# Optimization experiments

Measured on AMD Instinct MI355X. Metric: run time of the kernel, lower is better.

The kernel has to match this reference:

```python
import jax, jax.numpy as jnp
import numpy as np

N_QUBITS = 10
N_LAYERS = 4
DIM = 1 << N_QUBITS            # 1024
N3 = 3 * N_QUBITS              # params per rotation layer
N_PARAM = N3 * (N_LAYERS + 1)  # 150
BATCH = 8192

_C64 = jnp.complex64


def _rx(t):
    c = jnp.cos(t / 2).astype(_C64)
    s = jnp.sin(t / 2).astype(_C64)
    return jnp.stack([jnp.stack([c, -1j * s]), jnp.stack([-1j * s, c])])


def _ry(t):
    c = jnp.cos(t / 2).astype(_C64)
    s = jnp.sin(t / 2).astype(_C64)
    return jnp.stack([jnp.stack([c, -s]), jnp.stack([s, c])])


def _rz(t):
    e = jnp.exp(-1j * t.astype(_C64) / 2)
    z = jnp.zeros((), _C64)
    return jnp.stack([jnp.stack([e, z]), jnp.stack([z, jnp.conj(e)])])


def _apply1(state, gate, wire):
    """Apply a 2x2 gate to qubit `wire` of state [B, 2, ..., 2]."""
    axis = wire + 1  # axis 0 is batch
    s = jnp.moveaxis(state, axis, -1)
    s = jnp.einsum('ij,...j->...i', gate, s)
    return jnp.moveaxis(s, -1, axis)


def _cnot(state, ctrl, tgt):
    a, b = ctrl + 1, tgt + 1
    s = jnp.moveaxis(state, (a, b), (-2, -1))  # [..., ctrl, tgt]
    s = jnp.stack([s[..., 0, :], s[..., 1, ::-1]], axis=-2)
    return jnp.moveaxis(s, (-2, -1), (a, b))


def setup_inputs() -> dict:
    key = jax.random.key(0)
    k1, k2 = jax.random.split(key)
    x = jax.random.normal(k1, (BATCH, DIM), dtype=jnp.float32)
    he_std = (2.0 ** 0.5) * (5.0 ** -0.5)  # gain * 5^-0.5, w_mul with lrmul=1
    weight = jax.random.uniform(k2, (N_PARAM,), minval=0.0,
                                maxval=2.0 * np.pi, dtype=jnp.float32) * he_std
    return {"x": x, "weight": weight}


def reference(x, weight):
    # encoding layer: L2-normalize then cast to complex amplitudes
    norm = jnp.linalg.norm(x, axis=-1, keepdims=True)
    s = (x / jnp.maximum(norm, 1e-12)).astype(_C64)
    s = s.reshape((x.shape[0],) + (2,) * N_QUBITS)

    for l in range(N_LAYERS):
        w = weight[l * N3:(l + 1) * N3]
        # XYZ layer: Rx, then Ry, then Rz on every qubit
        for q in range(N_QUBITS):
            s = _apply1(s, _rx(w[q]), q)
        for q in range(N_QUBITS):
            s = _apply1(s, _ry(w[N_QUBITS + q]), q)
        for q in range(N_QUBITS):
            s = _apply1(s, _rz(w[2 * N_QUBITS + q]), q)
        # ring of CNOTs
        for q in range(N_QUBITS):
            s = _cnot(s, q, (q + 1) % N_QUBITS)

    # final YZY layer
    w = weight[N_LAYERS * N3:]
    for q in range(N_QUBITS):
        s = _apply1(s, _ry(w[q]), q)
    for q in range(N_QUBITS):
        s = _apply1(s, _rz(w[N_QUBITS + q]), q)
    for q in range(N_QUBITS):
        s = _apply1(s, _ry(w[2 * N_QUBITS + q]), q)

    return s.reshape(x.shape[0], 1, DIM).real
```

## Files before the change

kernel.cpp:

```cpp
#include <hip/hip_runtime.h>
#include <stdint.h>

typedef uint16_t u16;
typedef __attribute__((ext_vector_type(2))) float f32x2;
typedef __attribute__((ext_vector_type(4))) float f32x4;
typedef __attribute__((ext_vector_type(8))) short short8;
typedef __attribute__((ext_vector_type(4))) float float4v;
typedef __attribute__((ext_vector_type(4))) uint16_t u16x4;
typedef __attribute__((ext_vector_type(8))) uint16_t u16x8;

#define DIMQ 1024
#define BATCH 8192
#define KDIM 1024
#define NDIM 1024

#define RDL(v, l) __int_as_float(__builtin_amdgcn_readlane(__float_as_int(v), (l)))

__device__ __forceinline__ u16 f2bf(float f) {
  uint32_t u = __float_as_uint(f);
  u += 0x7fffu + ((u >> 16) & 1u);
  return (u16)(u >> 16);
}

template<int MASK>
__device__ __forceinline__ float lane_xor(float x) {
  if constexpr (MASK == 1)
    return __int_as_float(__builtin_amdgcn_update_dpp(0, __float_as_int(x), 0xB1, 0xF, 0xF, true));
  else if constexpr (MASK == 2)
    return __int_as_float(__builtin_amdgcn_update_dpp(0, __float_as_int(x), 0x4E, 0xF, 0xF, true));
  else if constexpr (MASK == 8)
    return __int_as_float(__builtin_amdgcn_update_dpp(0, __float_as_int(x), 0x128, 0xF, 0xF, true));
  else if constexpr (MASK == 4)
    return __int_as_float(__builtin_amdgcn_ds_swizzle(__float_as_int(x), 0x101F));
  else if constexpr (MASK == 16)
    return __int_as_float(__builtin_amdgcn_ds_swizzle(__float_as_int(x), 0x401F));
  else
    return __shfl_xor(x, 32, 64);
}

template<int MASK>
__device__ __forceinline__ void lane_gate8(float* ar, float* ai, int lane,
    float u00r, float u00i, float u01r, float u01i,
    float u10r, float u10i, float u11r, float u11i) {
  bool hi = (lane & MASK) != 0;
  float cmr = hi ? u11r : u00r, cmi = hi ? u11i : u00i;
  float cor = hi ? u10r : u01r, coi = hi ? u10i : u01i;
  float otr[8], oti[8];
#pragma unroll
  for (int r = 0; r < 8; ++r) otr[r] = lane_xor<MASK>(ar[r]);
#pragma unroll
  for (int r = 0; r < 8; ++r) oti[r] = lane_xor<MASK>(ai[r]);
#pragma unroll
  for (int k = 0; k < 4; ++k) {
    f32x2 A = {ar[2*k], ar[2*k+1]}, I = {ai[2*k], ai[2*k+1]};
    f32x2 R = {otr[2*k], otr[2*k+1]}, J = {oti[2*k], oti[2*k+1]};
    f32x2 nr = A*cmr - I*cmi + R*cor - J*coi;
    f32x2 ni = I*cmr + A*cmi + J*cor + R*coi;
    ar[2*k] = nr[0]; ar[2*k+1] = nr[1];
    ai[2*k] = ni[0]; ai[2*k+1] = ni[1];
  }
}

__device__ __forceinline__ void bfly2(f32x2 &a0r, f32x2 &a0i, f32x2 &a1r, f32x2 &a1i,
    float u00r, float u00i, float u01r, float u01i,
    float u10r, float u10i, float u11r, float u11i) {
  f32x2 t0r = a0r*u00r - a0i*u00i + a1r*u01r - a1i*u01i;
  f32x2 t0i = a0i*u00r + a0r*u00i + a1i*u01r + a1r*u01i;
  f32x2 t1r = a0r*u10r - a0i*u10i + a1r*u11r - a1i*u11i;
  f32x2 t1i = a0i*u10r + a0r*u10i + a1i*u11r + a1r*u11i;
  a0r = t0r; a0i = t0i; a1r = t1r; a1i = t1i;
}

__device__ inline void cmul2x2(float* O, const float* A, const float* B) {
  for (int r = 0; r < 2; ++r)
    for (int c = 0; c < 2; ++c) {
      float re = 0.f, im = 0.f;
      for (int j = 0; j < 2; ++j) {
        float ar = A[(r*2+j)*2], ai = A[(r*2+j)*2+1];
        float br = B[(j*2+c)*2], bi = B[(j*2+c)*2+1];
        re += ar*br - ai*bi;
        im += ar*bi + ai*br;
      }
      O[(r*2+c)*2]   = re;
      O[(r*2+c)*2+1] = im;
    }
}
__device__ inline void mk_rx(float* m, float t) {
  float s, c; sincosf(0.5f*t, &s, &c);
  m[0]=c; m[1]=0; m[2]=0; m[3]=-s; m[4]=0; m[5]=-s; m[6]=c; m[7]=0;
}
__device__ inline void mk_ry(float* m, float t) {
  float s, c; sincosf(0.5f*t, &s, &c);
  m[0]=c; m[1]=0; m[2]=-s; m[3]=0; m[4]=s; m[5]=0; m[6]=c; m[7]=0;
}
__device__ inline void mk_rz(float* m, float t) {
  float s, c; sincosf(0.5f*t, &s, &c);
  m[0]=c; m[1]=-s; m[2]=0; m[3]=0; m[4]=0; m[5]=0; m[6]=c; m[7]=s;
}

__device__ __forceinline__ int padi(int y) { return y + (y >> 4); }

__device__ __forceinline__ void do_stage(int gbase, float (&ar)[8], float (&ai)[8],
    f32x2* __restrict__ slab,
    const int (&idP0)[8], const int (&idP1)[8],
    int wbase, int lane, int h,
    float O0, float O1, float O2, float O3,
    float O4, float O5, float O6, float O7) {
  __syncthreads();
#pragma unroll
  for (int j = 0; j < 8; ++j) slab[wbase + j] = (f32x2){ar[j], ai[j]};
  __syncthreads();
  {
    int g = gbase + 6;
    float c0r = h ? RDL(O4,g) : RDL(O0,g), c0i = h ? RDL(O5,g) : RDL(O1,g);
    float c1r = h ? RDL(O6,g) : RDL(O2,g), c1i = h ? RDL(O7,g) : RDL(O3,g);
    f32x2 v0[8], v1[8];
#pragma unroll
    for (int j = 0; j < 8; ++j) {
      v0[j] = slab[idP0[j]];
      v1[j] = slab[idP1[j]];
    }
#pragma unroll
    for (int k = 0; k < 4; ++k) {
      f32x2 Vr0 = {v0[2*k][0], v0[2*k+1][0]}, Vi0 = {v0[2*k][1], v0[2*k+1][1]};
      f32x2 Vr1 = {v1[2*k][0], v1[2*k+1][0]}, Vi1 = {v1[2*k][1], v1[2*k+1][1]};
      f32x2 nr = Vr0*c0r - Vi0*c0i + Vr1*c1r - Vi1*c1i;
      f32x2 ni = Vi0*c0r + Vr0*c0i + Vi1*c1r + Vr1*c1i;
      ar[2*k] = nr[0]; ar[2*k+1] = nr[1];
      ai[2*k] = ni[0]; ai[2*k+1] = ni[1];
    }
  }
  { int g = gbase + 7;
    float u0r=RDL(O0,g),u0i=RDL(O1,g),u1r=RDL(O2,g),u1i=RDL(O3,g);
    float u2r=RDL(O4,g),u2i=RDL(O5,g),u3r=RDL(O6,g),u3i=RDL(O7,g);
    f32x2 a0r={ar[0],ar[1]}, a0i={ai[0],ai[1]}, a1r={ar[4],ar[5]}, a1i={ai[4],ai[5]};
    bfly2(a0r,a0i,a1r,a1i, u0r,u0i,u1r,u1i,u2r,u2i,u3r,u3i);
    ar[0]=a0r[0];ar[1]=a0r[1];ai[0]=a0i[0];ai[1]=a0i[1];
    ar[4]=a1r[0];ar[5]=a1r[1];ai[4]=a1i[0];ai[5]=a1i[1];
    f32x2 b0r={ar[2],ar[3]}, b0i={ai[2],ai[3]}, b1r={ar[6],ar[7]}, b1i={ai[6],ai[7]};
    bfly2(b0r,b0i,b1r,b1i, u0r,u0i,u1r,u1i,u2r,u2i,u3r,u3i);
    ar[2]=b0r[0];ar[3]=b0r[1];ai[2]=b0i[0];ai[3]=b0i[1];
    ar[6]=b1r[0];ar[7]=b1r[1];ai[6]=b1i[0];ai[7]=b1i[1];
  }
  { int g = gbase + 8;
    float u0r=RDL(O0,g),u0i=RDL(O1,g),u1r=RDL(O2,g),u1i=RDL(O3,g);
    float u2r=RDL(O4,g),u2i=RDL(O5,g),u3r=RDL(O6,g),u3i=RDL(O7,g);
    f32x2 a0r={ar[0],ar[1]}, a0i={ai[0],ai[1]}, a1r={ar[2],ar[3]}, a1i={ai[2],ai[3]};
    bfly2(a0r,a0i,a1r,a1i, u0r,u0i,u1r,u1i,u2r,u2i,u3r,u3i);
    ar[0]=a0r[0];ar[1]=a0r[1];ai[0]=a0i[0];ai[1]=a0i[1];
    ar[2]=a1r[0];ar[3]=a1r[1];ai[2]=a1i[0];ai[3]=a1i[1];
    f32x2 b0r={ar[4],ar[5]}, b0i={ai[4],ai[5]}, b1r={ar[6],ar[7]}, b1i={ai[6],ai[7]};
    bfly2(b0r,b0i,b1r,b1i, u0r,u0i,u1r,u1i,u2r,u2i,u3r,u3i);
    ar[4]=b0r[0];ar[5]=b0r[1];ai[4]=b0i[0];ai[5]=b0i[1];
    ar[6]=b1r[0];ar[7]=b1r[1];ai[6]=b1i[0];ai[7]=b1i[1];
  }
  { int g = gbase + 9;
    float u0r=RDL(O0,g),u0i=RDL(O1,g),u1r=RDL(O2,g),u1i=RDL(O3,g);
    float u2r=RDL(O4,g),u2i=RDL(O5,g),u3r=RDL(O6,g),u3i=RDL(O7,g);
    f32x2 a0r={ar[0],ar[2]}, a0i={ai[0],ai[2]}, a1r={ar[1],ar[3]}, a1i={ai[1],ai[3]};
    bfly2(a0r,a0i,a1r,a1i, u0r,u0i,u1r,u1i,u2r,u2i,u3r,u3i);
    ar[0]=a0r[0];ar[2]=a0r[1];ai[0]=a0i[0];ai[2]=a0i[1];
    ar[1]=a1r[0];ar[3]=a1r[1];ai[1]=a1i[0];ai[3]=a1i[1];
    f32x2 b0r={ar[4],ar[6]}, b0i={ai[4],ai[6]}, b1r={ar[5],ar[7]}, b1i={ai[5],ai[7]};
    bfly2(b0r,b0i,b1r,b1i, u0r,u0i,u1r,u1i,u2r,u2i,u3r,u3i);
    ar[4]=b0r[0];ar[6]=b0r[1];ai[4]=b0i[0];ai[6]=b0i[1];
    ar[5]=b1r[0];ar[7]=b1r[1];ai[5]=b1i[0];ai[7]=b1i[1];
  }
  { int g = gbase + 0; lane_gate8<32>(ar, ai, lane, RDL(O0,g),RDL(O1,g),RDL(O2,g),RDL(O3,g),RDL(O4,g),RDL(O5,g),RDL(O6,g),RDL(O7,g)); }
  { int g = gbase + 1; lane_gate8<16>(ar, ai, lane, RDL(O0,g),RDL(O1,g),RDL(O2,g),RDL(O3,g),RDL(O4,g),RDL(O5,g),RDL(O6,g),RDL(O7,g)); }
  { int g = gbase + 2; lane_gate8< 8>(ar, ai, lane, RDL(O0,g),RDL(O1,g),RDL(O2,g),RDL(O3,g),RDL(O4,g),RDL(O5,g),RDL(O6,g),RDL(O7,g)); }
  { int g = gbase + 3; lane_gate8< 4>(ar, ai, lane, RDL(O0,g),RDL(O1,g),RDL(O2,g),RDL(O3,g),RDL(O4,g),RDL(O5,g),RDL(O6,g),RDL(O7,g)); }
  { int g = gbase + 4; lane_gate8< 2>(ar, ai, lane, RDL(O0,g),RDL(O1,g),RDL(O2,g),RDL(O3,g),RDL(O4,g),RDL(O5,g),RDL(O6,g),RDL(O7,g)); }
  { int g = gbase + 5; lane_gate8< 1>(ar, ai, lane, RDL(O0,g),RDL(O1,g),RDL(O2,g),RDL(O3,g),RDL(O4,g),RDL(O5,g),RDL(O6,g),RDL(O7,g)); }
}

__global__ __launch_bounds__(256) void fused_front(const float* __restrict__ x,
                                                   const float* __restrict__ w,
                                                   u16* __restrict__ Abf,
                                                   u16* __restrict__ Bmat) {
  __shared__ f32x2 slab[2][1088];
  const int bid = blockIdx.x;
  const int lane = threadIdx.x & 63, wv = threadIdx.x >> 6;

  if (bid >= 512) {
    int base = (bid - 512) * 16 + wv * 4;
    for (int it = 0; it < 4; ++it) {
      int row = base + it;
      const float* xr = x + (size_t)row * DIMQ;
      float4v v[4];
      float ss = 0.f;
#pragma unroll
      for (int j = 0; j < 4; ++j) {
        v[j] = *(const float4v*)(xr + j*256 + lane*4);
        ss += v[j][0]*v[j][0] + v[j][1]*v[j][1] + v[j][2]*v[j][2] + v[j][3]*v[j][3];
      }
#pragma unroll
      for (int off = 32; off; off >>= 1) ss += __shfl_xor(ss, off, 64);
      float inv = 1.0f / fmaxf(sqrtf(ss), 1e-12f);
      u16* orow = Abf + (size_t)row * DIMQ;
#pragma unroll
      for (int j = 0; j < 4; ++j) {
        u16x4 o;
#pragma unroll
        for (int e = 0; e < 4; ++e) o[e] = f2bf(v[j][e] * inv);
        *(u16x4*)(orow + j*256 + lane*4) = o;
      }
    }
    return;
  }

  const int s = wv >> 1, h = wv & 1;
  const int d = bid * 2 + s;

  float O0, O1, O2, O3, O4, O5, O6, O7;
  {
    float A[8], B[8], C[8], T8[8], O[8];
    int t = lane;
    if (t < 50) {
      if (t < 10) {
        mk_ry(A, -w[120 + t]);
        mk_rz(B, -w[130 + t]);
        mk_ry(C, -w[140 + t]);
      } else {
        int sg = (t - 10) / 10, q = (t - 10) % 10, l = 3 - sg;
        mk_rx(A, -w[l*30 + q]);
        mk_ry(B, -w[l*30 + 10 + q]);
        mk_rz(C, -w[l*30 + 20 + q]);
      }
      cmul2x2(T8, A, B);
      cmul2x2(O, T8, C);
    } else {
#pragma unroll
      for (int j = 0; j < 8; ++j) O[j] = 0.f;
    }
    O0=O[0]; O1=O[1]; O2=O[2]; O3=O[3]; O4=O[4]; O5=O[5]; O6=O[6]; O7=O[7];
  }

  int idP0[8], idP1[8];
  int s8;
  {
    int yy = 8;
#pragma unroll
    for (int qq = 0; qq < 9; ++qq) yy ^= ((yy >> (9 - qq)) & 1) << (8 - qq);
    yy ^= (yy & 1) << 9;
    s8 = yy;
  }
#pragma unroll
  for (int j = 0; j < 8; ++j) {
    int xx = (lane << 4) + j;
    int yy = xx;
#pragma unroll
    for (int qq = 0; qq < 9; ++qq) yy ^= ((yy >> (9 - qq)) & 1) << (8 - qq);
    yy ^= (yy & 1) << 9;
    idP0[j] = padi(yy);
    idP1[j] = padi(yy ^ s8);
  }
  const int wbase = lane * 17 + h * 8;

  float ar[8], ai[8];
  {
    float fr = 1.0f, fi = 0.0f;
#pragma unroll
    for (int p = 4; p <= 9; ++p) {
      const int q = 9 - p;
      int c = (d >> p) & 1;
      float a0r = c ? RDL(O2,q) : RDL(O0,q), a0i = c ? RDL(O3,q) : RDL(O1,q);
      float a1r = c ? RDL(O6,q) : RDL(O4,q), a1i = c ? RDL(O7,q) : RDL(O5,q);
      bool hb = (lane >> (p - 4)) & 1;
      float gr = hb ? a1r : a0r, gi = hb ? a1i : a0i;
      float nr = fr*gr - fi*gi, ni = fr*gi + fi*gr;
      fr = nr; fi = ni;
    }
    {
      int c = (d >> 3) & 1;
      float a0r = c ? RDL(O2,6) : RDL(O0,6), a0i = c ? RDL(O3,6) : RDL(O1,6);
      float a1r = c ? RDL(O6,6) : RDL(O4,6), a1i = c ? RDL(O7,6) : RDL(O5,6);
      float gr = h ? a1r : a0r, gi = h ? a1i : a0i;
      float nr = fr*gr - fi*gi, ni = fr*gi + fi*gr;
      fr = nr; fi = ni;
    }
    float t2r[2], t2i[2], t1r[2], t1i[2], t0r[2], t0i[2];
    {
      int c = (d >> 2) & 1;
      t2r[0] = c ? RDL(O2,7) : RDL(O0,7); t2i[0] = c ? RDL(O3,7) : RDL(O1,7);
      t2r[1] = c ? RDL(O6,7) : RDL(O4,7); t2i[1] = c ? RDL(O7,7) : RDL(O5,7);
    }
    {
      int c = (d >> 1) & 1;
      t1r[0] = c ? RDL(O2,8) : RDL(O0,8); t1i[0] = c ? RDL(O3,8) : RDL(O1,8);
      t1r[1] = c ? RDL(O6,8) : RDL(O4,8); t1i[1] = c ? RDL(O7,8) : RDL(O5,8);
    }
    {
      int c = d & 1;
      t0r[0] = c ? RDL(O2,9) : RDL(O0,9); t0i[0] = c ? RDL(O3,9) : RDL(O1,9);
      t0r[1] = c ? RDL(O6,9) : RDL(O4,9); t0i[1] = c ? RDL(O7,9) : RDL(O5,9);
    }
    float m21r[4], m21i[4];
#pragma unroll
    for (int b2 = 0; b2 < 2; ++b2)
#pragma unroll
      for (int b1 = 0; b1 < 2; ++b1) {
        m21r[b2*2+b1] = t2r[b2]*t1r[b1] - t2i[b2]*t1i[b1];
        m21i[b2*2+b1] = t2r[b2]*t1i[b1] + t2i[b2]*t1r[b1];
      }
#pragma unroll
    for (int j = 0; j < 8; ++j) {
      int hi2 = j >> 1;
      int b0 = j & 1;
      float wr = m21r[hi2]*t0r[b0] - m21i[hi2]*t0i[b0];
      float wi = m21r[hi2]*t0i[b0] + m21i[hi2]*t0r[b0];
      ar[j] = fr*wr - fi*wi;
      ai[j] = fr*wi + fi*wr;
    }
  }

#pragma clang loop unroll(disable)
  for (int stage = 1; stage < 5; ++stage)
    do_stage(stage*10, ar, ai, slab[s], idP0, idP1, wbase, lane, h,
             O0,O1,O2,O3,O4,O5,O6,O7);

  u16x8 o;
#pragma unroll
  for (int j = 0; j < 8; ++j) o[j] = f2bf(ar[j]);
  *(u16x8*)(Bmat + (size_t)d * DIMQ + lane*16 + h*8) = o;
}

__global__ __launch_bounds__(256) void gemm_bt(const u16* __restrict__ A,
                                               const u16* __restrict__ Bm,
                                               float* __restrict__ C) {
  __shared__ u16 As[128*32];
  __shared__ u16 Bs[128*32];
  int t = threadIdx.x, lane = t & 63, wave = t >> 6;
  int bid = blockIdx.x;
  int nid = ((bid & 7) << 6) | (bid >> 3);
  int bm = nid >> 3, bn = nid & 7;
  size_t aBase = (size_t)bm * 128 * KDIM;
  size_t bBase = (size_t)bn * 128 * KDIM;
  int r0 = wave*16 + (lane >> 2);
  int c0 = (lane & 3) * 8;
  int wm = (wave >> 1) * 64, wn = (wave & 1) * 64;
  int la = lane & 15, lk = (lane >> 4) * 8;
  f32x4 acc[4][4];
#pragma unroll
  for (int m = 0; m < 4; ++m)
#pragma unroll
    for (int n = 0; n < 4; ++n) acc[m][n] = (f32x4){0.f, 0.f, 0.f, 0.f};

  for (int k0 = 0; k0 < KDIM; k0 += 32) {
    __syncthreads();
#pragma unroll
    for (int j = 0; j < 2; ++j) {
      __builtin_amdgcn_global_load_lds(
          (const __attribute__((address_space(1))) void*)(A + aBase + (size_t)(j*64 + r0)*KDIM + k0 + c0),
          (__attribute__((address_space(3))) void*)((char*)As + j*4096 + wave*1024), 16, 0, 0);
      __builtin_amdgcn_global_load_lds(
          (const __attribute__((address_space(1))) void*)(Bm + bBase + (size_t)(j*64 + r0)*KDIM + k0 + c0),
          (__attribute__((address_space(3))) void*)((char*)Bs + j*4096 + wave*1024), 16, 0, 0);
    }
    __syncthreads();
    short8 af[4], bf[4];
#pragma unroll
    for (int m = 0; m < 4; ++m) af[m] = *(const short8*)&As[(wm + m*16 + la)*32 + lk];
#pragma unroll
    for (int n = 0; n < 4; ++n) bf[n] = *(const short8*)&Bs[(wn + n*16 + la)*32 + lk];
#pragma unroll
    for (int m = 0; m < 4; ++m)
#pragma unroll
      for (int n = 0; n < 4; ++n)
        acc[m][n] = __builtin_amdgcn_mfma_f32_16x16x32_bf16(af[m], bf[n], acc[m][n], 0, 0, 0);
  }

  int orow0 = bm*128 + wm + (lane >> 4)*4;
  int ocol0 = bn*128 + wn + la;
#pragma unroll
  for (int m = 0; m < 4; ++m)
#pragma unroll
    for (int n = 0; n < 4; ++n)
#pragma unroll
      for (int j = 0; j < 4; ++j)
        C[(size_t)(orow0 + m*16 + j)*NDIM + ocol0 + n*16] = acc[m][n][j];
}

extern "C" void kernel_launch(void* const* d_in, const int* in_sizes, int n_in,
                              void* d_out, int out_size, void* d_ws, size_t ws_size,
                              hipStream_t stream) {
  const float* x = (const float*)d_in[0];
  const float* w = (const float*)d_in[1];
  float* out = (float*)d_out;
  char* ws = (char*)d_ws;
  u16* Bmat = (u16*)(ws + 4096);
  u16* Abf  = (u16*)(ws + 4096 + 2*1024*1024);

  fused_front<<<1024, 256, 0, stream>>>(x, w, Abf, Bmat);
  gemm_bt<<<(BATCH/128)*(NDIM/128), 256, 0, stream>>>(Abf, Bmat, out);
}
```

Baseline: 57.84 us.

## Double-buffer GEMM with larger 256x128 tiles, XOR-swizzled LDS, 512 threads

Rewrites the bf16 GEMM to use 256x128 block tiles with 8 waves, K-step 64, and double-buffered LDS. The next tile's global-to-LDS load is issued before the current tile's MFMAs, so load latency can overlap with compute. Reads and writes use an XOR swizzle to avoid LDS bank conflicts, and s_setprio raises priority around the MFMA block. Fewer, larger blocks (256 instead of 512) give more data reuse but lower the block count per CU and use more LDS (96KB) and registers.

```diff
diff --git a/kernel.cpp b/kernel.cpp
--- a/kernel.cpp
+++ b/kernel.cpp
@@ -325,57 +325,90 @@
   *(u16x8*)(Bmat + (size_t)d * DIMQ + lane*16 + h*8) = o;
 }
 
-__global__ __launch_bounds__(256) void gemm_bt(const u16* __restrict__ A,
+__global__ __launch_bounds__(512) void gemm_bt(const u16* __restrict__ A,
                                                const u16* __restrict__ Bm,
                                                float* __restrict__ C) {
-  __shared__ u16 As[128*32];
-  __shared__ u16 Bs[128*32];
-  int t = threadIdx.x, lane = t & 63, wave = t >> 6;
+  __shared__ u16 As[2][256*64];
+  __shared__ u16 Bs[2][128*64];
+  const int t = threadIdx.x, lane = t & 63, wave = t >> 6;
   int bid = blockIdx.x;
-  int nid = ((bid & 7) << 6) | (bid >> 3);
-  int bm = nid >> 3, bn = nid & 7;
-  size_t aBase = (size_t)bm * 128 * KDIM;
-  size_t bBase = (size_t)bn * 128 * KDIM;
-  int r0 = wave*16 + (lane >> 2);
-  int c0 = (lane & 3) * 8;
-  int wm = (wave >> 1) * 64, wn = (wave & 1) * 64;
-  int la = lane & 15, lk = (lane >> 4) * 8;
-  f32x4 acc[4][4];
-#pragma unroll
-  for (int m = 0; m < 4; ++m)
-#pragma unroll
-    for (int n = 0; n < 4; ++n) acc[m][n] = (f32x4){0.f, 0.f, 0.f, 0.f};
-
-  for (int k0 = 0; k0 < KDIM; k0 += 32) {
-    __syncthreads();
+  int nid = ((bid & 7) << 5) | (bid >> 3);
+  const int bm = nid >> 3, bn = nid & 7;
+  const size_t aBase = (size_t)bm * 256 * KDIM;
+  const size_t bBase = (size_t)bn * 128 * KDIM;
+
+  const int srow = t >> 3;
+  const int scol = ((t & 7) ^ (srow & 7)) * 8;
+  const int dstB = srow * 128 + (t & 7) * 16;
+
+  const int wm = wave >> 2, wn = wave & 3;
+  const int la = lane & 15;
+  const int lkB = ((lane >> 4) * 16);
+  const int rsw = (lane & 7) << 4;
+
+  f32x4 acc[8][2];
+#pragma unroll
+  for (int m = 0; m < 8; ++m)
+#pragma unroll
+    for (int n = 0; n < 2; ++n) acc[m][n] = (f32x4){0.f, 0.f, 0.f, 0.f};
+
+  auto stage = [&](int b, int kt) {
+    int k0 = kt * 64;
+#pragma unroll
+    for (int j = 0; j < 4; ++j) {
+      __builtin_amdgcn_global_load_lds(
+          (const __attribute__((address_space(1))) void*)(A + aBase + (size_t)(j*64 + srow)*KDIM + k0 + scol),
+          (__attribute__((address_space(3))) void*)((char*)&As[b][0] + j*8192 + dstB), 16, 0, 0);
+    }
 #pragma unroll
     for (int j = 0; j < 2; ++j) {
       __builtin_amdgcn_global_load_lds(
-          (const __attribute__((address_space(1))) void*)(A + aBase + (size_t)(j*64 + r0)*KDIM + k0 + c0),
-          (__attribute__((address_space(3))) void*)((char*)As + j*4096 + wave*1024), 16, 0, 0);
-      __builtin_amdgcn_global_load_lds(
-          (const __attribute__((address_space(1))) void*)(Bm + bBase + (size_t)(j*64 + r0)*KDIM + k0 + c0),
-          (__attribute__((address_space(3))) void*)((char*)Bs + j*4096 + wave*1024), 16, 0, 0);
-    }
+          (const __attribute__((address_space(1))) void*)(Bm + bBase + (size_t)(j*64 + srow)*KDIM + k0 + scol),
+          (__attribute__((address_space(3))) void*)((char*)&Bs[b][0] + j*8192 + dstB), 16, 0, 0);
+    }
+  };
+
+  stage(0, 0);
+  __syncthreads();
+
+  int cur = 0;
+  for (int kt = 0; kt < 16; ++kt) {
+    if (kt < 15) stage(cur ^ 1, kt + 1);
+    short8 af[8][2], bf[2][2];
+#pragma unroll
+    for (int kk = 0; kk < 2; ++kk) {
+#pragma unroll
+      for (int m = 0; m < 8; ++m) {
+        int row = wm*128 + m*16 + la;
+        int byt = (row*128 + kk*64 + lkB) ^ rsw;
+        af[m][kk] = *(const short8*)((char*)&As[cur][0] + byt);
+      }
+#pragma unroll
+      for (int n = 0; n < 2; ++n) {
+        int row = wn*32 + n*16 + la;
+        int byt = (row*128 + kk*64 + lkB) ^ rsw;
+        bf[n][kk] = *(const short8*)((char*)&Bs[cur][0] + byt);
+      }
+    }
+    __builtin_amdgcn_s_setprio(1);
+#pragma unroll
+    for (int kk = 0; kk < 2; ++kk)
+#pragma unroll
+      for (int m = 0; m < 8; ++m)
+#pragma unroll
+        for (int n = 0; n < 2; ++n)
+          acc[m][n] = __builtin_amdgcn_mfma_f32_16x16x32_bf16(af[m][kk], bf[n][kk], acc[m][n], 0, 0, 0);
+    __builtin_amdgcn_s_setprio(0);
     __syncthreads();
-    short8 af[4], bf[4];
-#pragma unroll
-    for (int m = 0; m < 4; ++m) af[m] = *(const short8*)&As[(wm + m*16 + la)*32 + lk];
-#pragma unroll
-    for (int n = 0; n < 4; ++n) bf[n] = *(const short8*)&Bs[(wn + n*16 + la)*32 + lk];
-#pragma unroll
-    for (int m = 0; m < 4; ++m)
-#pragma unroll
-      for (int n = 0; n < 4; ++n)
-        acc[m][n] = __builtin_amdgcn_mfma_f32_16x16x32_bf16(af[m], bf[n], acc[m][n], 0, 0, 0);
-  }
-
-  int orow0 = bm*128 + wm + (lane >> 4)*4;
-  int ocol0 = bn*128 + wn + la;
-#pragma unroll
-  for (int m = 0; m < 4; ++m)
-#pragma unroll
-    for (int n = 0; n < 4; ++n)
+    cur ^= 1;
+  }
+
+  int orow0 = bm*256 + wm*128 + (lane >> 4)*4;
+  int ocol0 = bn*128 + wn*32 + la;
+#pragma unroll
+  for (int m = 0; m < 8; ++m)
+#pragma unroll
+    for (int n = 0; n < 2; ++n)
 #pragma unroll
       for (int j = 0; j < 4; ++j)
         C[(size_t)(orow0 + m*16 + j)*NDIM + ocol0 + n*16] = acc[m][n][j];
@@ -392,5 +425,5 @@
   u16* Abf  = (u16*)(ws + 4096 + 2*1024*1024);
 
   fused_front<<<1024, 256, 0, stream>>>(x, w, Abf, Bmat);
-  gemm_bt<<<(BATCH/128)*(NDIM/128), 256, 0, stream>>>(Abf, Bmat, out);
-}
+  gemm_bt<<<(BATCH/256)*(NDIM/128), 512, 0, stream>>>(Abf, Bmat, out);
+}
```

New measurement: 56.09 us. -3.0%, faster.
